# Kernel tuning notes

Hardware: AMD Instinct MI355X
Metric: run time of the kernel (lower is better)

Reference implementation:

```python
import jax, jax.numpy as jnp
import numpy as np


def _haar_coeffs(x, s):
    # 2x2 depthwise Haar conv at stride s, no padding.
    # Output spatial size = floor((H-2)/s)+1 = len(range(0, H-1, s)).
    H, W = x.shape[-2], x.shape[-1]
    x00 = x[..., 0:H - 1:s, 0:W - 1:s]
    x01 = x[..., 0:H - 1:s, 1:W:s]
    x10 = x[..., 1:H:s, 0:W - 1:s]
    x11 = x[..., 1:H:s, 1:W:s]
    ll = (x00 + x01 + x10 + x11) * 0.25
    lh = (x00 + x01 - x10 - x11) * 0.25
    hl = (x00 - x01 + x10 - x11) * 0.25
    hh = (x00 - x01 - x10 + x11) * 0.25
    return ll, lh, hl, hh


def _resize_hw(x, H, W):
    # bilinear, half-pixel centers == torch align_corners=False (upsampling)
    return jax.image.resize(x, x.shape[:-2] + (H, W), method='linear')


def setup_inputs() -> dict:
    key = jax.random.key(0)
    x = jax.random.normal(key, (8, 64, 256, 256), dtype=jnp.float32)
    return {"x": x, "level": 2}


def reference(x, level):
    B, C, H, W = x.shape
    low_freq = x
    high_freq = jnp.zeros_like(x)
    for l in range(level):
        stride = 2 ** l
        if H // stride < 2 or W // stride < 2:
            break
        ll, lh, hl, hh = _haar_coeffs(low_freq, stride)
        current_high = jnp.abs(lh) + jnp.abs(hl) + jnp.abs(hh)
        high_freq = high_freq + _resize_hw(current_high, H, W)
        low_freq = _resize_hw(ll, H, W)
    if level > 0:
        high_freq = high_freq / level
    return (low_freq, high_freq)
```

## Files before the change

kernel.cpp:

```cpp
#include <hip/hip_runtime.h>


constexpr int IH = 256, IW = 256;
constexpr int TILE = 64;
constexpr int XT = 70;
constexpr int LT = 69;
constexpr int CT = 65;
constexpr int FT = 68;
constexpr int QT = 34;

__global__ __launch_bounds__(256)
void haar_fused(const float* __restrict__ x,
                float* __restrict__ out_low,
                float* __restrict__ out_high) {
  const int bc = blockIdx.y;
  const int ti = blockIdx.x >> 2;
  const int tj = blockIdx.x & 3;
  const int i0 = ti * TILE, j0 = tj * TILE;
  const int tid = threadIdx.x;

  __shared__ float sX[XT * XT];
  __shared__ float sLL1[LT * LT];
  __shared__ float sCH1[CT * CT];
  __shared__ float sLL2[QT * QT];
  __shared__ float sCH2[QT * QT];

  const float* xc = x + (size_t)bc * (IH * IW);

  for (int idx = tid; idx < XT * XT; idx += 256) {
    int r = idx / XT, c = idx - r * XT;
    int gr = min(max(i0 - 3 + r, 0), IH - 1);
    int gc = min(max(j0 - 3 + c, 0), IW - 1);
    sX[idx] = xc[gr * IW + gc];
  }
  __syncthreads();

  for (int idx = tid; idx < LT * LT; idx += 256) {
    int r = idx / LT, c = idx - r * LT;
    float x00 = sX[r * XT + c];
    float x01 = sX[r * XT + c + 1];
    float x10 = sX[(r + 1) * XT + c];
    float x11 = sX[(r + 1) * XT + c + 1];
    sLL1[idx] = 0.25f * (x00 + x01 + x10 + x11);
  }
  for (int idx = tid; idx < CT * CT; idx += 256) {
    int r = idx / CT, c = idx - r * CT;
    int xr = r + 2, xcol = c + 2;
    float x00 = sX[xr * XT + xcol];
    float x01 = sX[xr * XT + xcol + 1];
    float x10 = sX[(xr + 1) * XT + xcol];
    float x11 = sX[(xr + 1) * XT + xcol + 1];
    float sa = x00 + x01, sb = x10 + x11;
    float da = x00 - x01, db = x10 - x11;
    float lh = 0.25f * (sa - sb);
    float hl = 0.25f * (da + db);
    float hh = 0.25f * (da - db);
    sCH1[idx] = fabsf(lh) + fabsf(hl) + fabsf(hh);
  }
  __syncthreads();

  for (int idx = tid; idx < FT * FT; idx += 256) {
    int r = idx / FT, c = idx - r * FT;
    int R = i0 - 2 + r, C = j0 - 2 + c;
    float cr = (R + 0.5f) * (255.0f / 256.0f) - 0.5f;
    cr = fminf(fmaxf(cr, 0.0f), 254.0f);
    int a0 = (int)cr; if (a0 > 253) a0 = 253;
    float fr = cr - (float)a0;
    float cc = (C + 0.5f) * (255.0f / 256.0f) - 0.5f;
    cc = fminf(fmaxf(cc, 0.0f), 254.0f);
    int b0 = (int)cc; if (b0 > 253) b0 = 253;
    float fc = cc - (float)b0;
    int rs = a0 - (i0 - 3), cs = b0 - (j0 - 3);
    float v00 = sLL1[rs * LT + cs],       v01 = sLL1[rs * LT + cs + 1];
    float v10 = sLL1[(rs + 1) * LT + cs], v11 = sLL1[(rs + 1) * LT + cs + 1];
    float top = v00 + fc * (v01 - v00);
    float bot = v10 + fc * (v11 - v10);
    sX[idx] = top + fr * (bot - top);
  }
  __syncthreads();

  for (int idx = tid; idx < QT * QT; idx += 256) {
    int pr = idx / QT, pc = idx - pr * QT;
    float f00 = sX[(2 * pr) * FT + 2 * pc];
    float f01 = sX[(2 * pr) * FT + 2 * pc + 1];
    float f10 = sX[(2 * pr + 1) * FT + 2 * pc];
    float f11 = sX[(2 * pr + 1) * FT + 2 * pc + 1];
    float sa = f00 + f01, sb = f10 + f11;
    float da = f00 - f01, db = f10 - f11;
    sLL2[idx] = 0.25f * (sa + sb);
    float lh = 0.25f * (sa - sb);
    float hl = 0.25f * (da + db);
    float hh = 0.25f * (da - db);
    sCH2[idx] = fabsf(lh) + fabsf(hl) + fabsf(hh);
  }
  __syncthreads();

  const int p0 = (i0 >> 1) - 1, q0 = (j0 >> 1) - 1;
  const size_t obase = (size_t)bc * (IH * IW);
  for (int idx = tid; idx < TILE * TILE; idx += 256) {
    int r = idx >> 6, c = idx & 63;
    int i = i0 + r, j = j0 + c;

    float cr1 = (i + 0.5f) * (255.0f / 256.0f) - 0.5f;
    cr1 = fminf(fmaxf(cr1, 0.0f), 254.0f);
    int a0 = (int)cr1; if (a0 > 253) a0 = 253;
    float fr1 = cr1 - (float)a0;
    float cc1 = (j + 0.5f) * (255.0f / 256.0f) - 0.5f;
    cc1 = fminf(fmaxf(cc1, 0.0f), 254.0f);
    int b0 = (int)cc1; if (b0 > 253) b0 = 253;
    float fc1 = cc1 - (float)b0;
    int rs = a0 - (i0 - 1), cs = b0 - (j0 - 1);
    float h00 = sCH1[rs * CT + cs],       h01 = sCH1[rs * CT + cs + 1];
    float h10 = sCH1[(rs + 1) * CT + cs], h11 = sCH1[(rs + 1) * CT + cs + 1];
    float ht = h00 + fc1 * (h01 - h00);
    float hb = h10 + fc1 * (h11 - h10);
    float hi1 = ht + fr1 * (hb - ht);

    float cr2 = 0.5f * (float)i - 0.25f;
    cr2 = fminf(fmaxf(cr2, 0.0f), 127.0f);
    int p = (int)cr2; if (p > 126) p = 126;
    float fr2 = cr2 - (float)p;
    float cc2 = 0.5f * (float)j - 0.25f;
    cc2 = fminf(fmaxf(cc2, 0.0f), 127.0f);
    int q = (int)cc2; if (q > 126) q = 126;
    float fc2 = cc2 - (float)q;
    int ps = p - p0, qs = q - q0;

    float g00 = sCH2[ps * QT + qs],       g01 = sCH2[ps * QT + qs + 1];
    float g10 = sCH2[(ps + 1) * QT + qs], g11 = sCH2[(ps + 1) * QT + qs + 1];
    float gt = g00 + fc2 * (g01 - g00);
    float gb = g10 + fc2 * (g11 - g10);
    float hi2 = gt + fr2 * (gb - gt);

    float l00 = sLL2[ps * QT + qs],       l01 = sLL2[ps * QT + qs + 1];
    float l10 = sLL2[(ps + 1) * QT + qs], l11 = sLL2[(ps + 1) * QT + qs + 1];
    float lt = l00 + fc2 * (l01 - l00);
    float lb = l10 + fc2 * (l11 - l10);
    float lo = lt + fr2 * (lb - lt);

    out_low[obase + (size_t)i * IW + j] = lo;
    out_high[obase + (size_t)i * IW + j] = 0.5f * (hi1 + hi2);
  }
}

extern "C" void kernel_launch(void* const* d_in, const int* in_sizes, int n_in,
                              void* d_out, int out_size, void* d_ws, size_t ws_size,
                              hipStream_t stream) {
  (void)in_sizes; (void)n_in; (void)d_ws; (void)ws_size; (void)out_size;
  const float* x = (const float*)d_in[0];
  float* out_low = (float*)d_out;
  float* out_high = out_low + (size_t)8 * 64 * 256 * 256;

  dim3 grid(16, 512, 1);
  dim3 block(256, 1, 1);
  haar_fused<<<grid, block, 0, stream>>>(x, out_low, out_high);
}
```

Measured before the change: 483.2 us.

## Vectorize global loads/stores and restructure Haar stages as row-sliding passes

The tile load now uses aligned float4 global reads into a padded 72-wide shared buffer, with a fix-up pass for clamped edge columns. Stage 1 and the first resize become per-wave column sweeps that reuse the previous row's sums and interpolants, and the interpolation weights are computed in closed form. The final output stage processes four contiguous columns per thread and writes float4 to both outputs. This aims to cut global transaction count, integer division and redundant shared-memory reads, but adds edge-handling logic and more registers per thread.

Result: faster. 442.2 us (-8.5%).

```diff
diff --git a/kernel.cpp b/kernel.cpp
--- a/kernel.cpp
+++ b/kernel.cpp
@@ -1,13 +1,11 @@
 #include <hip/hip_runtime.h>
 
 
-constexpr int IH = 256, IW = 256;
-constexpr int TILE = 64;
-constexpr int XT = 70;
-constexpr int LT = 69;
-constexpr int CT = 65;
-constexpr int FT = 68;
-constexpr int QT = 34;
+constexpr int IW = 256, IH = 256;
+
+__device__ __forceinline__ float lerpf(float a, float b, float t) {
+  return a + t * (b - a);
+}
 
 __global__ __launch_bounds__(256)
 void haar_fused(const float* __restrict__ x,
@@ -16,130 +14,207 @@
   const int bc = blockIdx.y;
   const int ti = blockIdx.x >> 2;
   const int tj = blockIdx.x & 3;
-  const int i0 = ti * TILE, j0 = tj * TILE;
+  const int i0 = ti * 64, j0 = tj * 64;
   const int tid = threadIdx.x;
-
-  __shared__ float sX[XT * XT];
-  __shared__ float sLL1[LT * LT];
-  __shared__ float sCH1[CT * CT];
-  __shared__ float sLL2[QT * QT];
-  __shared__ float sCH2[QT * QT];
+  const int lane = tid & 63;
+  const int wid = tid >> 6;
+  const float c512 = 1.0f / 512.0f;
+
+  __shared__ float sX[70 * 72];
+  __shared__ float sLL1[69 * 69];
+  __shared__ float sCH1[65 * 65];
+  __shared__ float sLL2[34 * 34];
+  __shared__ float sCH2[34 * 34];
 
   const float* xc = x + (size_t)bc * (IH * IW);
 
-  for (int idx = tid; idx < XT * XT; idx += 256) {
-    int r = idx / XT, c = idx - r * XT;
-    int gr = min(max(i0 - 3 + r, 0), IH - 1);
-    int gc = min(max(j0 - 3 + c, 0), IW - 1);
-    sX[idx] = xc[gr * IW + gc];
-  }
-  __syncthreads();
-
-  for (int idx = tid; idx < LT * LT; idx += 256) {
-    int r = idx / LT, c = idx - r * LT;
-    float x00 = sX[r * XT + c];
-    float x01 = sX[r * XT + c + 1];
-    float x10 = sX[(r + 1) * XT + c];
-    float x11 = sX[(r + 1) * XT + c + 1];
-    sLL1[idx] = 0.25f * (x00 + x01 + x10 + x11);
-  }
-  for (int idx = tid; idx < CT * CT; idx += 256) {
-    int r = idx / CT, c = idx - r * CT;
-    int xr = r + 2, xcol = c + 2;
-    float x00 = sX[xr * XT + xcol];
-    float x01 = sX[xr * XT + xcol + 1];
-    float x10 = sX[(xr + 1) * XT + xcol];
-    float x11 = sX[(xr + 1) * XT + xcol + 1];
-    float sa = x00 + x01, sb = x10 + x11;
-    float da = x00 - x01, db = x10 - x11;
-    float lh = 0.25f * (sa - sb);
-    float hl = 0.25f * (da + db);
-    float hh = 0.25f * (da - db);
-    sCH1[idx] = fabsf(lh) + fabsf(hl) + fabsf(hh);
-  }
-  __syncthreads();
-
-  for (int idx = tid; idx < FT * FT; idx += 256) {
-    int r = idx / FT, c = idx - r * FT;
-    int R = i0 - 2 + r, C = j0 - 2 + c;
-    float cr = (R + 0.5f) * (255.0f / 256.0f) - 0.5f;
-    cr = fminf(fmaxf(cr, 0.0f), 254.0f);
-    int a0 = (int)cr; if (a0 > 253) a0 = 253;
-    float fr = cr - (float)a0;
-    float cc = (C + 0.5f) * (255.0f / 256.0f) - 0.5f;
-    cc = fminf(fmaxf(cc, 0.0f), 254.0f);
-    int b0 = (int)cc; if (b0 > 253) b0 = 253;
-    float fc = cc - (float)b0;
-    int rs = a0 - (i0 - 3), cs = b0 - (j0 - 3);
-    float v00 = sLL1[rs * LT + cs],       v01 = sLL1[rs * LT + cs + 1];
-    float v10 = sLL1[(rs + 1) * LT + cs], v11 = sLL1[(rs + 1) * LT + cs + 1];
-    float top = v00 + fc * (v01 - v00);
-    float bot = v10 + fc * (v11 - v10);
-    sX[idx] = top + fr * (bot - top);
-  }
-  __syncthreads();
-
-  for (int idx = tid; idx < QT * QT; idx += 256) {
-    int pr = idx / QT, pc = idx - pr * QT;
-    float f00 = sX[(2 * pr) * FT + 2 * pc];
-    float f01 = sX[(2 * pr) * FT + 2 * pc + 1];
-    float f10 = sX[(2 * pr + 1) * FT + 2 * pc];
-    float f11 = sX[(2 * pr + 1) * FT + 2 * pc + 1];
+  const int colbase = min(max(j0 - 4, 0), IW - 72);
+  const int soff = colbase - j0 + 4;
+  for (int idx = tid; idx < 70 * 18; idx += 256) {
+    int r = idx / 18;
+    int c4 = idx - r * 18;
+    int gslot = 4 * c4 + soff;
+    if (gslot >= 0 && gslot <= 68) {
+      int gr = min(max(i0 - 3 + r, 0), IH - 1);
+      const float4 v = *reinterpret_cast<const float4*>(&xc[gr * IW + colbase + 4 * c4]);
+      *reinterpret_cast<float4*>(&sX[r * 72 + gslot]) = v;
+    }
+  }
+  if (soff != 0) {
+    __syncthreads();
+    if (tid < 70) {
+      if (soff > 0) {
+        float v = sX[tid * 72 + 4];
+        sX[tid * 72 + 0] = v; sX[tid * 72 + 1] = v;
+        sX[tid * 72 + 2] = v; sX[tid * 72 + 3] = v;
+      } else {
+        float v = sX[tid * 72 + 67];
+        sX[tid * 72 + 68] = v; sX[tid * 72 + 69] = v;
+        sX[tid * 72 + 70] = v; sX[tid * 72 + 71] = v;
+      }
+    }
+  }
+  __syncthreads();
+
+  {
+    int r0 = wid * 18;
+    int r1 = min(r0 + 18, 69);
+    int xc0 = lane + 1;
+    float a = sX[r0 * 72 + xc0], b = sX[r0 * 72 + xc0 + 1];
+    float s = a + b, d = a - b;
+    for (int xr = r0; xr < r1; ++xr) {
+      float a2 = sX[(xr + 1) * 72 + xc0], b2 = sX[(xr + 1) * 72 + xc0 + 1];
+      float s2 = a2 + b2, d2 = a2 - b2;
+      sLL1[xr * 69 + lane] = 0.25f * (s + s2);
+      float lh = 0.25f * (s - s2);
+      float hl = 0.25f * (d + d2);
+      float hh = 0.25f * (d - d2);
+      float ch = fabsf(lh) + fabsf(hl) + fabsf(hh);
+      if (lane >= 2 && (unsigned)(xr - 2) <= 64u)
+        sCH1[(xr - 2) * 65 + (lane - 2)] = ch;
+      s = s2; d = d2;
+    }
+  }
+  for (int f = tid; f < 5 * 69; f += 256) {
+    int q = f / 69;
+    int xr = f - q * 69;
+    int xc0 = 65 + q;
+    float a = sX[xr * 72 + xc0], b = sX[xr * 72 + xc0 + 1];
+    float a2 = sX[(xr + 1) * 72 + xc0], b2 = sX[(xr + 1) * 72 + xc0 + 1];
+    float s = a + b, d = a - b, s2 = a2 + b2, d2 = a2 - b2;
+    sLL1[xr * 69 + (xc0 - 1)] = 0.25f * (s + s2);
+    if (xc0 <= 67 && (unsigned)(xr - 2) <= 64u) {
+      float lh = 0.25f * (s - s2);
+      float hl = 0.25f * (d + d2);
+      float hh = 0.25f * (d - d2);
+      sCH1[(xr - 2) * 65 + (xc0 - 3)] = fabsf(lh) + fabsf(hl) + fabsf(hh);
+    }
+  }
+  __syncthreads();
+
+  {
+    int fcc = lane;
+    int C = j0 - 2 + fcc;
+    float ccf = (float)C - (float)(2 * C + 1) * c512;
+    float fc = fminf(fmaxf(ccf, 0.0f), 254.0f) - (float)(C - 1);
+    int r0 = wid * 17, r1 = r0 + 17;
+    float A = sLL1[r0 * 69 + fcc], B = sLL1[r0 * 69 + fcc + 1];
+    float hz = A + fc * (B - A);
+    for (int fr = r0; fr < r1; ++fr) {
+      float A2 = sLL1[(fr + 1) * 69 + fcc], B2 = sLL1[(fr + 1) * 69 + fcc + 1];
+      float hz2 = A2 + fc * (B2 - A2);
+      int R = i0 - 2 + fr;
+      float crf = (float)R - (float)(2 * R + 1) * c512;
+      float fw = fminf(fmaxf(crf, 0.0f), 254.0f) - (float)(R - 1);
+      sX[fr * 68 + fcc] = hz + fw * (hz2 - hz);
+      hz = hz2;
+    }
+  }
+  for (int f = tid; f < 4 * 68; f += 256) {
+    int q = f / 68;
+    int fr = f - q * 68;
+    int fcc = 64 + q;
+    int C = j0 - 2 + fcc;
+    float ccf = (float)C - (float)(2 * C + 1) * c512;
+    float fc = fminf(fmaxf(ccf, 0.0f), 254.0f) - (float)(C - 1);
+    float A = sLL1[fr * 69 + fcc], B = sLL1[fr * 69 + fcc + 1];
+    float A2 = sLL1[(fr + 1) * 69 + fcc], B2 = sLL1[(fr + 1) * 69 + fcc + 1];
+    int R = i0 - 2 + fr;
+    float crf = (float)R - (float)(2 * R + 1) * c512;
+    float fw = fminf(fmaxf(crf, 0.0f), 254.0f) - (float)(R - 1);
+    float hz = A + fc * (B - A);
+    float hz2 = A2 + fc * (B2 - A2);
+    sX[fr * 68 + fcc] = hz + fw * (hz2 - hz);
+  }
+  __syncthreads();
+
+  for (int idx = tid; idx < 34 * 32; idx += 256) {
+    int pr = idx >> 5, pc = idx & 31;
+    int base = (2 * pr) * 68 + 2 * pc;
+    float f00 = sX[base], f01 = sX[base + 1];
+    float f10 = sX[base + 68], f11 = sX[base + 69];
     float sa = f00 + f01, sb = f10 + f11;
     float da = f00 - f01, db = f10 - f11;
-    sLL2[idx] = 0.25f * (sa + sb);
-    float lh = 0.25f * (sa - sb);
-    float hl = 0.25f * (da + db);
-    float hh = 0.25f * (da - db);
-    sCH2[idx] = fabsf(lh) + fabsf(hl) + fabsf(hh);
-  }
-  __syncthreads();
-
-  const int p0 = (i0 >> 1) - 1, q0 = (j0 >> 1) - 1;
-  const size_t obase = (size_t)bc * (IH * IW);
-  for (int idx = tid; idx < TILE * TILE; idx += 256) {
-    int r = idx >> 6, c = idx & 63;
-    int i = i0 + r, j = j0 + c;
-
-    float cr1 = (i + 0.5f) * (255.0f / 256.0f) - 0.5f;
-    cr1 = fminf(fmaxf(cr1, 0.0f), 254.0f);
-    int a0 = (int)cr1; if (a0 > 253) a0 = 253;
-    float fr1 = cr1 - (float)a0;
-    float cc1 = (j + 0.5f) * (255.0f / 256.0f) - 0.5f;
-    cc1 = fminf(fmaxf(cc1, 0.0f), 254.0f);
-    int b0 = (int)cc1; if (b0 > 253) b0 = 253;
-    float fc1 = cc1 - (float)b0;
-    int rs = a0 - (i0 - 1), cs = b0 - (j0 - 1);
-    float h00 = sCH1[rs * CT + cs],       h01 = sCH1[rs * CT + cs + 1];
-    float h10 = sCH1[(rs + 1) * CT + cs], h11 = sCH1[(rs + 1) * CT + cs + 1];
-    float ht = h00 + fc1 * (h01 - h00);
-    float hb = h10 + fc1 * (h11 - h10);
-    float hi1 = ht + fr1 * (hb - ht);
-
-    float cr2 = 0.5f * (float)i - 0.25f;
-    cr2 = fminf(fmaxf(cr2, 0.0f), 127.0f);
-    int p = (int)cr2; if (p > 126) p = 126;
-    float fr2 = cr2 - (float)p;
-    float cc2 = 0.5f * (float)j - 0.25f;
-    cc2 = fminf(fmaxf(cc2, 0.0f), 127.0f);
-    int q = (int)cc2; if (q > 126) q = 126;
-    float fc2 = cc2 - (float)q;
-    int ps = p - p0, qs = q - q0;
-
-    float g00 = sCH2[ps * QT + qs],       g01 = sCH2[ps * QT + qs + 1];
-    float g10 = sCH2[(ps + 1) * QT + qs], g11 = sCH2[(ps + 1) * QT + qs + 1];
-    float gt = g00 + fc2 * (g01 - g00);
-    float gb = g10 + fc2 * (g11 - g10);
-    float hi2 = gt + fr2 * (gb - gt);
-
-    float l00 = sLL2[ps * QT + qs],       l01 = sLL2[ps * QT + qs + 1];
-    float l10 = sLL2[(ps + 1) * QT + qs], l11 = sLL2[(ps + 1) * QT + qs + 1];
-    float lt = l00 + fc2 * (l01 - l00);
-    float lb = l10 + fc2 * (l11 - l10);
-    float lo = lt + fr2 * (lb - lt);
-
-    out_low[obase + (size_t)i * IW + j] = lo;
-    out_high[obase + (size_t)i * IW + j] = 0.5f * (hi1 + hi2);
+    sLL2[pr * 34 + pc] = 0.25f * (sa + sb);
+    sCH2[pr * 34 + pc] =
+        fabsf(0.25f * (sa - sb)) + fabsf(0.25f * (da + db)) + fabsf(0.25f * (da - db));
+  }
+  if (tid < 68) {
+    int pr = tid >> 1, pc = 32 + (tid & 1);
+    int base = (2 * pr) * 68 + 2 * pc;
+    float f00 = sX[base], f01 = sX[base + 1];
+    float f10 = sX[base + 68], f11 = sX[base + 69];
+    float sa = f00 + f01, sb = f10 + f11;
+    float da = f00 - f01, db = f10 - f11;
+    sLL2[pr * 34 + pc] = 0.25f * (sa + sb);
+    sCH2[pr * 34 + pc] =
+        fabsf(0.25f * (sa - sb)) + fabsf(0.25f * (da + db)) + fabsf(0.25f * (da - db));
+  }
+  __syncthreads();
+
+  {
+    const int cg = tid & 15, rb = tid >> 4;
+    const int cbase = 4 * cg;
+    const int q0 = (j0 >> 1) - 1;
+    const int p0 = (i0 >> 1) - 1;
+    float fc1[4], fc2[4];
+#pragma unroll
+    for (int m = 0; m < 4; ++m) {
+      int jj = j0 + cbase + m;
+      float ccf = (float)jj - (float)(2 * jj + 1) * c512;
+      fc1[m] = fminf(fmaxf(ccf, 0.0f), 254.0f) - (float)(jj - 1);
+      int qu = (jj - 1) >> 1;
+      fc2[m] = fminf(fmaxf(0.5f * (float)jj - 0.25f, 0.0f), 127.0f) - (float)qu;
+    }
+    const int qs0 = ((j0 + cbase - 1) >> 1) - q0;
+    const size_t obase = (size_t)bc * (IH * IW);
+
+#pragma unroll
+    for (int k = 0; k < 4; ++k) {
+      int r = rb + 16 * k;
+      int i = i0 + r;
+      float crf = (float)i - (float)(2 * i + 1) * c512;
+      float fr1 = fminf(fmaxf(crf, 0.0f), 254.0f) - (float)(i - 1);
+      int pu = (i - 1) >> 1;
+      float fr2 = fminf(fmaxf(0.5f * (float)i - 0.25f, 0.0f), 127.0f) - (float)pu;
+      int ps = pu - p0;
+
+      const float* chA = &sCH1[r * 65 + cbase];
+      const float* chB = chA + 65;
+      const float* llA = &sLL2[ps * 34 + qs0];
+      const float* llB = llA + 34;
+      const float* c2A = &sCH2[ps * 34 + qs0];
+      const float* c2B = c2A + 34;
+
+      float av[5], bv[5];
+#pragma unroll
+      for (int m = 0; m < 5; ++m) { av[m] = chA[m]; bv[m] = chB[m]; }
+      float lav[4], lbv[4], gav[4], gbv[4];
+#pragma unroll
+      for (int m = 0; m < 4; ++m) {
+        lav[m] = llA[m]; lbv[m] = llB[m];
+        gav[m] = c2A[m]; gbv[m] = c2B[m];
+      }
+
+      float lo[4], hi[4];
+#pragma unroll
+      for (int m = 0; m < 4; ++m) {
+        const int k2 = (m == 0) ? 0 : (m == 3 ? 2 : 1);
+        float h1 = lerpf(lerpf(av[m], av[m + 1], fc1[m]),
+                         lerpf(bv[m], bv[m + 1], fc1[m]), fr1);
+        float l_ = lerpf(lerpf(lav[k2], lav[k2 + 1], fc2[m]),
+                         lerpf(lbv[k2], lbv[k2 + 1], fc2[m]), fr2);
+        float h2 = lerpf(lerpf(gav[k2], gav[k2 + 1], fc2[m]),
+                         lerpf(gbv[k2], gbv[k2 + 1], fc2[m]), fr2);
+        lo[m] = l_;
+        hi[m] = 0.5f * (h1 + h2);
+      }
+      float4 lowv = make_float4(lo[0], lo[1], lo[2], lo[3]);
+      float4 highv = make_float4(hi[0], hi[1], hi[2], hi[3]);
+      size_t off = obase + (size_t)i * IW + (j0 + cbase);
+      *reinterpret_cast<float4*>(&out_low[off]) = lowv;
+      *reinterpret_cast<float4*>(&out_high[off]) = highv;
+    }
   }
 }
 
```
